# Kernel optimization log

Measured on AMD Instinct MI355X. Metric: run time of the kernel, lower is better.

The kernel has to match this reference:

```python
import jax, jax.numpy as jnp
import numpy as np

N_NODES = 100000
N_EDGES = 1600000
D_IN = 128
D_OUT = 128
BN_EPS = 1e-5


def setup_inputs() -> dict:
    key = jax.random.key(0)
    ks = jax.random.split(key, 6)
    x = jax.random.normal(ks[0], (N_NODES, D_IN), dtype=jnp.float32)
    edge_index = jax.random.randint(ks[1], (2, N_EDGES), 0, N_NODES, dtype=jnp.int32)
    edge_weight = jax.random.uniform(ks[2], (N_EDGES,), dtype=jnp.float32)
    W = jax.random.normal(ks[3], (D_IN, D_OUT), dtype=jnp.float32) / np.sqrt(D_IN)
    b = jax.random.normal(ks[4], (D_OUT,), dtype=jnp.float32) * 0.01
    gamma = jnp.ones((D_OUT,), dtype=jnp.float32)
    beta = jnp.zeros((D_OUT,), dtype=jnp.float32)
    return {"x": x, "edge_index": edge_index, "edge_weight": edge_weight,
            "W": W, "b": b, "gamma": gamma, "beta": beta}


def reference(x, edge_index, edge_weight, W, b, gamma, beta):
    n = x.shape[0]
    # add self loops (add_self_loops=True)
    self_loops = jnp.arange(n, dtype=edge_index.dtype)
    row = jnp.concatenate([edge_index[0], self_loops])  # source
    col = jnp.concatenate([edge_index[1], self_loops])  # destination
    ew = jnp.concatenate([edge_weight, jnp.ones((n,), x.dtype)])
    # degree via scatter-add of ones on source nodes
    deg = jax.ops.segment_sum(jnp.ones_like(ew), row, num_segments=n)
    dinv = jnp.where(deg > 0, jax.lax.rsqrt(deg), 0.0)
    norm = dinv[row] * dinv[col] * ew  # [E+N]
    # linear transform
    h = x @ W + b  # [N, D_OUT]
    # per-edge gather -> scale -> scatter-add (vectorized form of the python loop)
    msgs = norm[:, None] * h[row]  # [E+N, D_OUT]
    out = jax.ops.segment_sum(msgs, col, num_segments=n)  # [N, D_OUT]
    # BatchNorm1d (training mode: biased batch stats)
    mean = jnp.mean(out, axis=0)
    var = jnp.mean(jnp.square(out - mean), axis=0)
    out = (out - mean) * jax.lax.rsqrt(var + BN_EPS) * gamma + beta
    return jax.nn.relu(out)
```

## Files before the change

kernel.cpp:

```cpp
#include <hip/hip_runtime.h>

#define DD 128
#define BINCAP 4608
#define S1_EPB 7168
#define DEG_R 16384
#define DEG_S 8

typedef __attribute__((ext_vector_type(8))) short short8;
typedef __attribute__((ext_vector_type(4))) float f32x4;

__device__ __forceinline__ unsigned short f2bf(float f) {
    unsigned int u; __builtin_memcpy(&u, &f, 4);
    unsigned int r = (u + 0x7FFFu + ((u >> 16) & 1u)) >> 16;
    return (unsigned short)r;
}
__device__ __forceinline__ unsigned int pack_bf(float a, float b) {
    return (unsigned int)f2bf(a) | ((unsigned int)f2bf(b) << 16);
}
__device__ __forceinline__ float lo_bf(unsigned int p) {
    unsigned int u = (p & 0xFFFFu) << 16; float f; __builtin_memcpy(&f, &u, 4); return f;
}
__device__ __forceinline__ float hi_bf(unsigned int p) {
    unsigned int u = p & 0xFFFF0000u; float f; __builtin_memcpy(&f, &u, 4); return f;
}
__device__ __forceinline__ float i2f(int v) { float f; __builtin_memcpy(&f, &v, 4); return f; }
__device__ __forceinline__ int f2i(float v) { int i; __builtin_memcpy(&i, &v, 4); return i; }

__global__ void k_prep(int* deg, int* cursor, float* colsumR, float* colsumsqR, int N, int NBIN,
                       int nInit, const float* __restrict__ W, unsigned short* __restrict__ Wfrag) {
    int bid = blockIdx.x, t = threadIdx.x;
    if (bid < nInit) {
        int i = bid * 256 + t;
        if (i < N) deg[i] = 1;
        if (i < NBIN) cursor[i] = 0;
        if (i < 1024) { colsumR[i] = 0.0f; colsumsqR[i] = 0.0f; }
        return;
    }
    int i = (bid - nInit) * 256 + t;
    int k = i >> 7, n = i & 127;
    int tt = n >> 4, s = k >> 5, l = (((k >> 3) & 3) << 4) | (n & 15), j = k & 7;
    Wfrag[((tt * 4 + s) * 64 + l) * 8 + j] = f2bf(W[k * DD + n]);
}

__global__ __launch_bounds__(1024) void k_fused(
    const int* __restrict__ ei, const float* __restrict__ ew,
    int* __restrict__ deg, int* __restrict__ cursor, long long* __restrict__ coarse,
    int E, int N, int NBIN, int nS1i, int nDeg,
    const float* __restrict__ x, const unsigned short* __restrict__ Wfrag,
    const float* __restrict__ b, unsigned short* __restrict__ h)
{
    __shared__ int smem[16384];
    int t = threadIdx.x;
    int id = blockIdx.x;
    int role, rid;
    if (id < 2 * nS1i)           { role = (id & 1); rid = id >> 1; }
    else if (id < 2 * nS1i + nDeg) { role = 2; rid = id - 2 * nS1i; }
    else                         { role = 1; rid = nS1i + (id - 2 * nS1i - nDeg); }

    const int* row = ei;
    const int* col = ei + E;

    if (role == 0) {
        int* scnt  = smem;
        int* soff  = smem + 512;
        int* gbase = smem + 1024;
        long long* sorted = (long long*)(smem + 1536);
        for (int i = t; i < 512; i += 1024) scnt[i] = 0;
        __syncthreads();
        int e0 = rid * S1_EPB;
        int myrank[7];
#pragma unroll
        for (int j = 0; j < 7; ++j) {
            int e = e0 + j * 1024 + t;
            if (e < E) myrank[j] = atomicAdd(&scnt[col[e] >> 8], 1);
        }
        __syncthreads();
        if (t < 512) soff[t] = scnt[t];
        __syncthreads();
        for (int off = 1; off < 512; off <<= 1) {
            int v = 0;
            if (t < 512 && t >= off) v = soff[t - off];
            __syncthreads();
            if (t < 512) soff[t] += v;
            __syncthreads();
        }
        if (t < NBIN && scnt[t] > 0) gbase[t] = atomicAdd(&cursor[t], scnt[t]);
#pragma unroll
        for (int j = 0; j < 7; ++j) {
            int e = e0 + j * 1024 + t;
            if (e < E) {
                int c = col[e];
                int bn = c >> 8;
                int lo = row[e] | ((c & 255) << 17);
                long long ent = ((long long)(unsigned)f2i(ew[e]) << 32) | (unsigned)lo;
                sorted[(soff[bn] - scnt[bn]) + myrank[j]] = ent;
            }
        }
        __syncthreads();
        int wave = t >> 6, lane = t & 63;
        for (int bn = wave; bn < NBIN; bn += 16) {
            int k = scnt[bn];
            if (k == 0) continue;
            int off0 = soff[bn] - k;
            int gb = gbase[bn];
            long long* dst = coarse + (size_t)bn * BINCAP;
            for (int j = lane; j < k; j += 64) {
                int gp = gb + j;
                if (gp < BINCAP) dst[gp] = sorted[off0 + j];
            }
        }
        return;
    }
    if (role == 2) {
        int nr = (N + DEG_R - 1) / DEG_R;
        int ri = rid % nr, si = rid / nr;
        int* lc = smem;
        for (int i = t; i < DEG_R; i += 1024) lc[i] = 0;
        __syncthreads();
        int base = ri * DEG_R;
        int per = (E + DEG_S - 1) / DEG_S;
        int es = si * per, ee = es + per; if (ee > E) ee = E;
        int q0 = es >> 2, q1 = ee >> 2;
        const int4* r4 = (const int4*)row;
        for (int q = q0 + t; q < q1; q += 1024) {
            int4 v = r4[q];
            unsigned d0 = (unsigned)(v.x - base), d1 = (unsigned)(v.y - base);
            unsigned d2 = (unsigned)(v.z - base), d3 = (unsigned)(v.w - base);
            if (d0 < DEG_R) atomicAdd(&lc[d0], 1);
            if (d1 < DEG_R) atomicAdd(&lc[d1], 1);
            if (d2 < DEG_R) atomicAdd(&lc[d2], 1);
            if (d3 < DEG_R) atomicAdd(&lc[d3], 1);
        }
        for (int e = (q1 << 2) + t; e < ee; e += 1024) {
            unsigned d = (unsigned)(row[e] - base);
            if (d < DEG_R) atomicAdd(&lc[d], 1);
        }
        __syncthreads();
        for (int i = t; i < DEG_R; i += 1024) {
            int node = base + i, k = lc[i];
            if (node < N && k) atomicAdd(&deg[node], k);
        }
        return;
    }
    int lane = t & 63, wave = t >> 6;
    int row0 = rid * 256 + wave * 16;
    int mrow = row0 + (lane & 15);
    int kgrp = lane >> 4;
    f32x4 acc[8];
#pragma unroll
    for (int i = 0; i < 8; ++i) acc[i] = (f32x4){0.f, 0.f, 0.f, 0.f};
    const short8* Wf = (const short8*)Wfrag;
#pragma unroll
    for (int s = 0; s < 4; ++s) {
        float xv[8];
        if (mrow < N) {
            const float4* xp = (const float4*)(x + (size_t)mrow * DD + s * 32 + kgrp * 8);
            float4 xa = xp[0], xb = xp[1];
            xv[0] = xa.x; xv[1] = xa.y; xv[2] = xa.z; xv[3] = xa.w;
            xv[4] = xb.x; xv[5] = xb.y; xv[6] = xb.z; xv[7] = xb.w;
        } else {
#pragma unroll
            for (int j = 0; j < 8; ++j) xv[j] = 0.f;
        }
        short8 af;
#pragma unroll
        for (int j = 0; j < 8; ++j) af[j] = (short)f2bf(xv[j]);
#pragma unroll
        for (int tt = 0; tt < 8; ++tt) {
            short8 bf = Wf[(tt * 4 + s) * 64 + lane];
            acc[tt] = __builtin_amdgcn_mfma_f32_16x16x32_bf16(af, bf, acc[tt], 0, 0, 0);
        }
    }
    int drow = row0 + (lane >> 4) * 4;
    int coll = lane & 15;
#pragma unroll
    for (int tt = 0; tt < 8; ++tt) {
        int cc = tt * 16 + coll;
        float bias = b[cc];
#pragma unroll
        for (int rr = 0; rr < 4; ++rr) {
            int rw = drow + rr;
            if (rw < N) h[(size_t)rw * DD + cc] = f2bf(acc[tt][rr] + bias);
        }
    }
}

__global__ __launch_bounds__(1024) void k_agg(
    const long long* __restrict__ coarse, const int* __restrict__ cursor,
    const int* __restrict__ deg, const unsigned int* __restrict__ h,
    unsigned int* __restrict__ outb, float* __restrict__ colsumR,
    float* __restrict__ colsumsqR, int N)
{
    __shared__ long long sorted2[BINCAP];
    __shared__ int fcnt[256], fpos[256], fcur[256];
    __shared__ float ls[2048], lq[2048];
    int bn = blockIdx.x, t = threadIdx.x;
    int m = cursor[bn]; if (m > BINCAP) m = BINCAP;
    for (int i = t; i < 256; i += 1024) fcnt[i] = 0;
    __syncthreads();
    const long long* src = coarse + (size_t)bn * BINCAP;
    for (int i = t; i < m; i += 1024) {
        int lo = (int)src[i];
        atomicAdd(&fcnt[(lo >> 17) & 255], 1);
    }
    __syncthreads();
    if (t < 256) fpos[t] = fcnt[t];
    __syncthreads();
    for (int off = 1; off < 256; off <<= 1) {
        int v = 0;
        if (t < 256 && t >= off) v = fpos[t - off];
        __syncthreads();
        if (t < 256) fpos[t] += v;
        __syncthreads();
    }
    if (t < 256) fcur[t] = fpos[t] - fcnt[t];
    __syncthreads();
    for (int i = t; i < m; i += 1024) {
        long long v = src[i];
        int lo = (int)v;
        int clo = (lo >> 17) & 255;
        int sr = lo & 0x1FFFF;
        int c = (bn << 8) + clo;
        float w = rsqrtf((float)deg[sr]) * rsqrtf((float)deg[c]) * i2f((int)(v >> 32));
        int p = atomicAdd(&fcur[clo], 1);
        sorted2[p] = ((long long)(unsigned)f2i(w) << 32) | (unsigned)sr;
    }
    __syncthreads();
    int wave = t >> 6, lane = t & 63;
    float s0 = 0, s1 = 0, q0 = 0, q1 = 0;
    const int2* sp = (const int2*)sorted2;
    for (int d = wave; d < 256; d += 16) {
        int c = (bn << 8) + d;
        if (c >= N) continue;
        float dn = rsqrtf((float)deg[c]);
        float sn = dn * dn;
        unsigned int p = h[(size_t)c * 64 + lane];
        float a0 = sn * lo_bf(p), a1 = sn * hi_bf(p);
        int cn = fcnt[d];
        int off0 = fpos[d] - cn;
        int j = 0;
        for (; j + 8 <= cn; j += 8) {
            int2 d0 = sp[off0 + j],     d1 = sp[off0 + j + 1];
            int2 d2 = sp[off0 + j + 2], d3 = sp[off0 + j + 3];
            int2 d4 = sp[off0 + j + 4], d5 = sp[off0 + j + 5];
            int2 d6 = sp[off0 + j + 6], d7 = sp[off0 + j + 7];
            unsigned int g0 = h[(size_t)d0.x * 64 + lane];
            unsigned int g1 = h[(size_t)d1.x * 64 + lane];
            unsigned int g2 = h[(size_t)d2.x * 64 + lane];
            unsigned int g3 = h[(size_t)d3.x * 64 + lane];
            unsigned int g4 = h[(size_t)d4.x * 64 + lane];
            unsigned int g5 = h[(size_t)d5.x * 64 + lane];
            unsigned int g6 = h[(size_t)d6.x * 64 + lane];
            unsigned int g7 = h[(size_t)d7.x * 64 + lane];
            float w0 = i2f(d0.y), w1 = i2f(d1.y), w2 = i2f(d2.y), w3 = i2f(d3.y);
            float w4 = i2f(d4.y), w5 = i2f(d5.y), w6 = i2f(d6.y), w7 = i2f(d7.y);
            a0 = fmaf(w0, lo_bf(g0), a0); a1 = fmaf(w0, hi_bf(g0), a1);
            a0 = fmaf(w1, lo_bf(g1), a0); a1 = fmaf(w1, hi_bf(g1), a1);
            a0 = fmaf(w2, lo_bf(g2), a0); a1 = fmaf(w2, hi_bf(g2), a1);
            a0 = fmaf(w3, lo_bf(g3), a0); a1 = fmaf(w3, hi_bf(g3), a1);
            a0 = fmaf(w4, lo_bf(g4), a0); a1 = fmaf(w4, hi_bf(g4), a1);
            a0 = fmaf(w5, lo_bf(g5), a0); a1 = fmaf(w5, hi_bf(g5), a1);
            a0 = fmaf(w6, lo_bf(g6), a0); a1 = fmaf(w6, hi_bf(g6), a1);
            a0 = fmaf(w7, lo_bf(g7), a0); a1 = fmaf(w7, hi_bf(g7), a1);
        }
        for (; j < cn; ++j) {
            int2 dd = sp[off0 + j];
            unsigned int g = h[(size_t)dd.x * 64 + lane];
            float w = i2f(dd.y);
            a0 = fmaf(w, lo_bf(g), a0);
            a1 = fmaf(w, hi_bf(g), a1);
        }
        outb[(size_t)c * 64 + lane] = pack_bf(a0, a1);
        s0 += a0; q0 += a0 * a0;
        s1 += a1; q1 += a1 * a1;
    }
    ls[wave * 128 + lane * 2] = s0; ls[wave * 128 + lane * 2 + 1] = s1;
    lq[wave * 128 + lane * 2] = q0; lq[wave * 128 + lane * 2 + 1] = q1;
    __syncthreads();
    if (t < 128) {
        float S = 0, Q = 0;
#pragma unroll
        for (int w = 0; w < 16; ++w) { S += ls[w * 128 + t]; Q += lq[w * 128 + t]; }
        int rep = (bn & 7) * 128 + t;
        atomicAdd(&colsumR[rep], S);
        atomicAdd(&colsumsqR[rep], Q);
    }
}

__global__ __launch_bounds__(256) void k_bn(
    const unsigned int* __restrict__ outb, float* __restrict__ out,
    const float* __restrict__ colsumR, const float* __restrict__ colsumsqR,
    const float* __restrict__ gamma, const float* __restrict__ beta,
    int N, int total64)
{
    __shared__ float ss[256];
    int t = threadIdx.x;
    if (t < 128) {
        float S = 0, Q = 0;
#pragma unroll
        for (int r = 0; r < 8; ++r) { S += colsumR[r * 128 + t]; Q += colsumsqR[r * 128 + t]; }
        float invN = 1.0f / (float)N;
        float mean = S * invN;
        float var = Q * invN - mean * mean;
        float inv = rsqrtf(var + 1e-5f);
        float sc = gamma[t] * inv;
        ss[t] = sc;
        ss[128 + t] = beta[t] - mean * sc;
    }
    __syncthreads();
    for (int i = blockIdx.x * 256 + t; i < total64; i += gridDim.x * 256) {
        int c0 = (i & 63) * 2;
        unsigned int p = outb[i];
        float v0 = fmaxf(lo_bf(p) * ss[c0]     + ss[128 + c0],     0.0f);
        float v1 = fmaxf(hi_bf(p) * ss[c0 + 1] + ss[128 + c0 + 1], 0.0f);
        ((float2*)out)[i] = make_float2(v0, v1);
    }
}

extern "C" void kernel_launch(void* const* d_in, const int* in_sizes, int n_in,
                              void* d_out, int out_size, void* d_ws, size_t ws_size,
                              hipStream_t stream) {
    const float* x     = (const float*)d_in[0];
    const int* ei      = (const int*)d_in[1];
    const float* ew    = (const float*)d_in[2];
    const float* W     = (const float*)d_in[3];
    const float* b     = (const float*)d_in[4];
    const float* gamma = (const float*)d_in[5];
    const float* beta  = (const float*)d_in[6];
    float* out = (float*)d_out;

    int N = in_sizes[0] / DD;
    int E = in_sizes[2];
    int NBIN = (N + 255) / 256;

    char* wsb = (char*)d_ws;
    size_t off = 0;
    auto alloc = [&](size_t bytes) -> char* {
        char* p = wsb + off;
        off = (off + bytes + 255) & ~(size_t)255;
        return p;
    };
    int* deg        = (int*)alloc((size_t)N * 4);
    int* cursor     = (int*)alloc((size_t)NBIN * 4);
    long long* coarse = (long long*)alloc((size_t)NBIN * BINCAP * 8);
    unsigned short* h = (unsigned short*)alloc((size_t)N * DD * 2);
    unsigned short* Wfrag = (unsigned short*)alloc(DD * DD * 2);
    unsigned int* outb = (unsigned int*)alloc((size_t)N * 64 * 4);
    float* colsumR   = (float*)alloc(1024 * 4);
    float* colsumsqR = (float*)alloc(1024 * 4);

    int nInit = (N + 255) / 256;
    int nS1   = (E + S1_EPB - 1) / S1_EPB;
    int nGemm = (N + 255) / 256;
    int nS1i  = (nS1 < nGemm) ? nS1 : nGemm;
    int nDeg  = ((N + DEG_R - 1) / DEG_R) * DEG_S;
    int GF    = 2 * nS1i + nDeg + (nGemm - nS1i);

    k_prep<<<dim3(nInit + 64), dim3(256), 0, stream>>>(deg, cursor, colsumR, colsumsqR,
                                                       N, NBIN, nInit, W, Wfrag);
    k_fused<<<dim3(GF), dim3(1024), 0, stream>>>(ei, ew, deg, cursor, coarse, E, N, NBIN,
                                                 nS1i, nDeg, x, Wfrag, b, h);
    k_agg<<<dim3(NBIN), dim3(1024), 0, stream>>>(coarse, cursor, deg, (const unsigned int*)h,
                                                 outb, colsumR, colsumsqR, N);
    k_bn<<<dim3(2048), dim3(256), 0, stream>>>(outb, out, colsumR, colsumsqR,
                                               gamma, beta, N, N * 64);
}
```

Before: 236.7 us.

## Stage GEMM output in LDS, vectorize BN, memset init, more degree splits

The GEMM epilogue now writes bf16 results into shared memory and then copies them out to h with coalesced 16-byte stores, replacing scattered 2-byte global stores. The BN kernel processes four columns per thread with uint2 loads and float4 stores, and its grid is halved. Zero-initialisation moves from a custom prep kernel to a single hipMemsetAsync over a contiguous region; the self-loop +1 is added at read time instead of initialising deg to 1. The number of degree-counting splits is doubled to raise parallelism, which adds more global atomics.

```diff
diff --git a/kernel.cpp b/kernel.cpp
--- a/kernel.cpp
+++ b/kernel.cpp
@@ -4,7 +4,7 @@
 #define BINCAP 4608
 #define S1_EPB 7168
 #define DEG_R 16384
-#define DEG_S 8
+#define DEG_S 16
 
 typedef __attribute__((ext_vector_type(8))) short short8;
 typedef __attribute__((ext_vector_type(4))) float f32x4;
@@ -26,17 +26,8 @@
 __device__ __forceinline__ float i2f(int v) { float f; __builtin_memcpy(&f, &v, 4); return f; }
 __device__ __forceinline__ int f2i(float v) { int i; __builtin_memcpy(&i, &v, 4); return i; }
 
-__global__ void k_prep(int* deg, int* cursor, float* colsumR, float* colsumsqR, int N, int NBIN,
-                       int nInit, const float* __restrict__ W, unsigned short* __restrict__ Wfrag) {
-    int bid = blockIdx.x, t = threadIdx.x;
-    if (bid < nInit) {
-        int i = bid * 256 + t;
-        if (i < N) deg[i] = 1;
-        if (i < NBIN) cursor[i] = 0;
-        if (i < 1024) { colsumR[i] = 0.0f; colsumsqR[i] = 0.0f; }
-        return;
-    }
-    int i = (bid - nInit) * 256 + t;
+__global__ void k_wprep(const float* __restrict__ W, unsigned short* __restrict__ Wfrag) {
+    int i = blockIdx.x * 256 + threadIdx.x;
     int k = i >> 7, n = i & 127;
     int tt = n >> 4, s = k >> 5, l = (((k >> 3) & 3) << 4) | (n & 15), j = k & 7;
     Wfrag[((tt * 4 + s) * 64 + l) * 8 + j] = f2bf(W[k * DD + n]);
@@ -143,7 +134,8 @@
         return;
     }
     int lane = t & 63, wave = t >> 6;
-    int row0 = rid * 256 + wave * 16;
+    int lrow0 = wave * 16;
+    int row0 = rid * 256 + lrow0;
     int mrow = row0 + (lane & 15);
     int kgrp = lane >> 4;
     f32x4 acc[8];
@@ -171,17 +163,23 @@
             acc[tt] = __builtin_amdgcn_mfma_f32_16x16x32_bf16(af, bf, acc[tt], 0, 0, 0);
         }
     }
-    int drow = row0 + (lane >> 4) * 4;
+    unsigned short* ht = (unsigned short*)smem;
+    int drowl = lrow0 + (lane >> 4) * 4;
     int coll = lane & 15;
 #pragma unroll
     for (int tt = 0; tt < 8; ++tt) {
-        int cc = tt * 16 + coll;
-        float bias = b[cc];
-#pragma unroll
-        for (int rr = 0; rr < 4; ++rr) {
-            int rw = drow + rr;
-            if (rw < N) h[(size_t)rw * DD + cc] = f2bf(acc[tt][rr] + bias);
-        }
+        float bias = b[tt * 16 + coll];
+#pragma unroll
+        for (int rr = 0; rr < 4; ++rr)
+            ht[(drowl + rr) * 128 + tt * 16 + coll] = f2bf(acc[tt][rr] + bias);
+    }
+    __syncthreads();
+    int lim = N - rid * 256;
+    const int4* hts = (const int4*)smem;
+    int4* hg = (int4*)(h + (size_t)rid * 256 * DD);
+    for (int i = t; i < 4096; i += 1024) {
+        int lr = i >> 4;
+        if (lr < lim) hg[i] = hts[i];
     }
 }
 
@@ -221,7 +219,7 @@
         int clo = (lo >> 17) & 255;
         int sr = lo & 0x1FFFF;
         int c = (bn << 8) + clo;
-        float w = rsqrtf((float)deg[sr]) * rsqrtf((float)deg[c]) * i2f((int)(v >> 32));
+        float w = rsqrtf((float)(deg[sr] + 1)) * rsqrtf((float)(deg[c] + 1)) * i2f((int)(v >> 32));
         int p = atomicAdd(&fcur[clo], 1);
         sorted2[p] = ((long long)(unsigned)f2i(w) << 32) | (unsigned)sr;
     }
@@ -232,7 +230,7 @@
     for (int d = wave; d < 256; d += 16) {
         int c = (bn << 8) + d;
         if (c >= N) continue;
-        float dn = rsqrtf((float)deg[c]);
+        float dn = rsqrtf((float)(deg[c] + 1));
         float sn = dn * dn;
         unsigned int p = h[(size_t)c * 64 + lane];
         float a0 = sn * lo_bf(p), a1 = sn * hi_bf(p);
@@ -291,7 +289,7 @@
     const unsigned int* __restrict__ outb, float* __restrict__ out,
     const float* __restrict__ colsumR, const float* __restrict__ colsumsqR,
     const float* __restrict__ gamma, const float* __restrict__ beta,
-    int N, int total64)
+    int N, int total32)
 {
     __shared__ float ss[256];
     int t = threadIdx.x;
@@ -308,12 +306,17 @@
         ss[128 + t] = beta[t] - mean * sc;
     }
     __syncthreads();
-    for (int i = blockIdx.x * 256 + t; i < total64; i += gridDim.x * 256) {
-        int c0 = (i & 63) * 2;
-        unsigned int p = outb[i];
-        float v0 = fmaxf(lo_bf(p) * ss[c0]     + ss[128 + c0],     0.0f);
-        float v1 = fmaxf(hi_bf(p) * ss[c0 + 1] + ss[128 + c0 + 1], 0.0f);
-        ((float2*)out)[i] = make_float2(v0, v1);
+    const uint2* ob = (const uint2*)outb;
+    float4* o4 = (float4*)out;
+    for (int i = blockIdx.x * 256 + t; i < total32; i += gridDim.x * 256) {
+        int c0 = (i & 31) * 4;
+        uint2 p = ob[i];
+        float4 v;
+        v.x = fmaxf(lo_bf(p.x) * ss[c0]     + ss[128 + c0],     0.0f);
+        v.y = fmaxf(hi_bf(p.x) * ss[c0 + 1] + ss[128 + c0 + 1], 0.0f);
+        v.z = fmaxf(lo_bf(p.y) * ss[c0 + 2] + ss[128 + c0 + 2], 0.0f);
+        v.w = fmaxf(hi_bf(p.y) * ss[c0 + 3] + ss[128 + c0 + 3], 0.0f);
+        o4[i] = v;
     }
 }
 
@@ -340,28 +343,29 @@
         off = (off + bytes + 255) & ~(size_t)255;
         return p;
     };
-    int* deg        = (int*)alloc((size_t)N * 4);
-    int* cursor     = (int*)alloc((size_t)NBIN * 4);
+    size_t zwords = (size_t)N + NBIN + 1024 + 1024;
+    int* zzone     = (int*)alloc(zwords * 4);
+    int* deg       = zzone;
+    int* cursor    = zzone + N;
+    float* colsumR   = (float*)(zzone + N + NBIN);
+    float* colsumsqR = colsumR + 1024;
     long long* coarse = (long long*)alloc((size_t)NBIN * BINCAP * 8);
     unsigned short* h = (unsigned short*)alloc((size_t)N * DD * 2);
     unsigned short* Wfrag = (unsigned short*)alloc(DD * DD * 2);
     unsigned int* outb = (unsigned int*)alloc((size_t)N * 64 * 4);
-    float* colsumR   = (float*)alloc(1024 * 4);
-    float* colsumsqR = (float*)alloc(1024 * 4);
-
-    int nInit = (N + 255) / 256;
+
     int nS1   = (E + S1_EPB - 1) / S1_EPB;
     int nGemm = (N + 255) / 256;
     int nS1i  = (nS1 < nGemm) ? nS1 : nGemm;
     int nDeg  = ((N + DEG_R - 1) / DEG_R) * DEG_S;
     int GF    = 2 * nS1i + nDeg + (nGemm - nS1i);
 
-    k_prep<<<dim3(nInit + 64), dim3(256), 0, stream>>>(deg, cursor, colsumR, colsumsqR,
-                                                       N, NBIN, nInit, W, Wfrag);
+    hipMemsetAsync(zzone, 0, zwords * 4, stream);
+    k_wprep<<<dim3(64), dim3(256), 0, stream>>>(W, Wfrag);
     k_fused<<<dim3(GF), dim3(1024), 0, stream>>>(ei, ew, deg, cursor, coarse, E, N, NBIN,
                                                  nS1i, nDeg, x, Wfrag, b, h);
     k_agg<<<dim3(NBIN), dim3(1024), 0, stream>>>(coarse, cursor, deg, (const unsigned int*)h,
                                                  outb, colsumR, colsumsqR, N);
-    k_bn<<<dim3(2048), dim3(256), 0, stream>>>(outb, out, colsumR, colsumsqR,
-                                               gamma, beta, N, N * 64);
-}
+    k_bn<<<dim3(1024), dim3(256), 0, stream>>>(outb, out, colsumR, colsumsqR,
+                                               gamma, beta, N, N * 32);
+}
```

Result: no change. 240.4 us (+1.6%).
